# Optimization experiments

Measured on AMD Instinct MI355X. Metric: run time of the kernel, lower is better.

Reference implementation:

```python
import jax, jax.numpy as jnp
import numpy as np
from jax import lax

B, S, D, H, K, FF = 8, 1024, 512, 8, 3, 1024
BUCKETS, MAX_REL = 32, 128
DH = D // H
SPAN = BUCKETS  # att_span when position_buckets > 0


def setup_inputs() -> dict:
    key = jax.random.key(0)
    ks = jax.random.split(key, 12)
    n = lambda k, shp, s=0.02: jax.random.normal(k, shp, jnp.float32) * s
    return dict(
        x=jax.random.normal(ks[0], (B, S, D), jnp.float32),
        ln1_g=jnp.ones((D,), jnp.float32), ln1_b=jnp.zeros((D,), jnp.float32),
        dw_w=n(ks[1], (D, 1, K), 0.1), dw_b=jnp.zeros((D,), jnp.float32),
        pw_w=n(ks[2], (D, D)), pw_b=jnp.zeros((D,), jnp.float32),
        ln2_g=jnp.ones((D,), jnp.float32), ln2_b=jnp.zeros((D,), jnp.float32),
        q_w=n(ks[3], (D, D)), q_b=jnp.zeros((D,), jnp.float32),
        k_w=n(ks[4], (D, D)), k_b=jnp.zeros((D,), jnp.float32),
        v_w=n(ks[5], (D, D)), v_b=jnp.zeros((D,), jnp.float32),
        o_w=n(ks[6], (D, D)), o_b=jnp.zeros((D,), jnp.float32),
        rel_emb=n(ks[7], (2 * SPAN, D)),
        ln3_g=jnp.ones((D,), jnp.float32), ln3_b=jnp.zeros((D,), jnp.float32),
        w1=n(ks[8], (FF, D)), b1=jnp.zeros((FF,), jnp.float32),
        w2=n(ks[9], (D, FF)), b2=jnp.zeros((D,), jnp.float32),
    )


def _ln(x, g, b):
    m = x.mean(-1, keepdims=True)
    v = jnp.var(x, axis=-1, keepdims=True)
    return (x - m) * lax.rsqrt(v + 1e-5) * g + b


def _rel_bucket():
    # DeBERTa-v2 log-bucket relative positions, [S, S] int32
    ids = jnp.arange(S, dtype=jnp.int32)
    rel = ids[:, None] - ids[None, :]
    mid = BUCKETS // 2
    sign = jnp.sign(rel)
    abs_pos = jnp.where((rel < mid) & (rel > -mid), mid - 1, jnp.abs(rel)).astype(jnp.float32)
    log_pos = jnp.ceil(jnp.log(abs_pos / mid) / np.log((MAX_REL - 1) / mid) * (mid - 1)) + mid
    return jnp.where(abs_pos <= mid, rel, (log_pos * sign).astype(jnp.int32)).astype(jnp.int32)


def _attention(x, q_w, q_b, k_w, k_b, v_w, v_b, o_w, o_b, rel_emb):
    def heads(t):  # [B,S,D] -> [B,H,S,DH]
        return t.reshape(B, S, H, DH).transpose(0, 2, 1, 3)

    q = heads(x @ q_w.T + q_b)
    k = heads(x @ k_w.T + k_b)
    v = heads(x @ v_w.T + v_b)
    scale = 1.0 / np.sqrt(DH * 3)  # scale_factor = 1 + len(['c2p','p2c'])

    scores = jnp.einsum('bhid,bhjd->bhij', q, k) * scale  # content-to-content

    rel = _rel_bucket()  # [S,S]
    # shared att key: project rel embeddings with same q/k projections -> [H, 2*SPAN, DH]
    pos_k = (rel_emb @ k_w.T + k_b).reshape(2 * SPAN, H, DH).transpose(1, 0, 2)
    pos_q = (rel_emb @ q_w.T + q_b).reshape(2 * SPAN, H, DH).transpose(1, 0, 2)

    # content-to-position
    c2p = jnp.einsum('bhid,hjd->bhij', q, pos_k)  # [B,H,S,2*SPAN]
    c2p_idx = jnp.clip(rel + SPAN, 0, 2 * SPAN - 1)[None, None]  # [1,1,S,S]
    scores = scores + jnp.take_along_axis(c2p, c2p_idx, axis=-1) * scale

    # position-to-content
    p2c = jnp.einsum('bhid,hjd->bhij', k, pos_q)  # [B,H,S,2*SPAN]
    p2c_idx = jnp.clip(-rel + SPAN, 0, 2 * SPAN - 1)[None, None]
    scores = scores + jnp.take_along_axis(p2c, p2c_idx, axis=-1).swapaxes(-1, -2) * scale

    probs = jax.nn.softmax(scores, axis=-1)
    ctx = jnp.einsum('bhij,bhjd->bhid', probs, v).transpose(0, 2, 1, 3).reshape(B, S, D)
    return ctx @ o_w.T + o_b


def reference(x, ln1_g, ln1_b, dw_w, dw_b, pw_w, pw_b, ln2_g, ln2_b,
              q_w, q_b, k_w, k_b, v_w, v_b, o_w, o_b, rel_emb,
              ln3_g, ln3_b, w1, b1, w2, b2):
    # conv block (pre-norm)
    res = x
    xn = _ln(x, ln1_g, ln1_b)
    xc = xn.transpose(0, 2, 1)  # [B,D,S]
    dw = lax.conv_general_dilated(xc, dw_w, (1,), [(K // 2, K // 2)],
                                  dimension_numbers=('NCH', 'OIH', 'NCH'),
                                  feature_group_count=D) + dw_b[None, :, None]
    pw = jnp.einsum('od,bds->bos', pw_w, jax.nn.silu(dw)) + pw_b[None, :, None]
    x = res + pw.transpose(0, 2, 1)
    # attention block
    res = x
    x = res + _attention(_ln(x, ln2_g, ln2_b), q_w, q_b, k_w, k_b, v_w, v_b, o_w, o_b, rel_emb)
    # FFN block
    res = x
    xn = _ln(x, ln3_g, ln3_b)
    ff = jax.nn.silu(xn @ w1.T + b1) @ w2.T + b2
    return res + ff
```

## Files before the change

kernel.cpp:

```cpp
#include <hip/hip_runtime.h>
#include <hip/hip_bf16.h>
#include <math.h>


#define B_  8
#define S_  1024
#define D_  512
#define H_  8
#define DH_ 64
#define FF_ 1024
#define BS_ (B_*S_)

typedef __attribute__((ext_vector_type(8))) short  short8;
typedef __attribute__((ext_vector_type(4))) short  short4v;
typedef __attribute__((ext_vector_type(4))) float  f32x4;
typedef __attribute__((ext_vector_type(4))) int    int4v;

static __device__ __forceinline__ float b2f(short u){
  union { int i; float f; } cv; cv.i = ((int)(unsigned short)u) << 16; return cv.f;
}
static __device__ __forceinline__ short f2b(float f){
  union { float f; unsigned u; } cv; cv.f = f;
  unsigned r = cv.u + 0x7FFFu + ((cv.u >> 16) & 1u);
  return (short)(r >> 16);
}
static __device__ __forceinline__ float silu_f(float x){
  return x / (1.f + __expf(-x));
}
static __device__ __forceinline__ f32x4 mfma16(short8 a, short8 b, f32x4 c){
  return __builtin_amdgcn_mfma_f32_16x16x32_bf16(a, b, c, 0, 0, 0);
}

struct F2B8 { const float* s[8]; short* d[8]; int n[8]; };
__global__ __launch_bounds__(256) void f2b8_kernel(F2B8 a){
  int seg = blockIdx.y;
  int i = (blockIdx.x*256 + threadIdx.x)*4;
  if (i >= a.n[seg]) return;
  float4 v = *(const float4*)(a.s[seg] + i);
  short4v o; o.x = f2b(v.x); o.y = f2b(v.y); o.z = f2b(v.z); o.w = f2b(v.w);
  *(short4v*)(a.d[seg] + i) = o;
}

__global__ __launch_bounds__(256) void tab_kernel(signed char* __restrict__ tab){
  int t = blockIdx.x*256 + threadIdx.x;
  if (t >= 2048) return;
  int d = t - 1023;
  int ad = d < 0 ? -d : d;
  int bkt;
  if (ad <= 16) bkt = d;
  else {
    const float inv_log = 15.f / logf(7.9375f);
    float lp = ceilf(logf((float)ad * (1.f/16.f)) * inv_log) + 16.f;
    int ilp = (int)lp;
    bkt = (d > 0) ? ilp : -ilp;
  }
  int idx = bkt + 32;
  idx = idx < 0 ? 0 : (idx > 63 ? 63 : idx);
  tab[t] = (signed char)idx;
}

__global__ __launch_bounds__(128) void ln_kernel(const float* __restrict__ x,
                                                 const float* __restrict__ g,
                                                 const float* __restrict__ bb,
                                                 short* __restrict__ out){
  int row = blockIdx.x;
  int tid = threadIdx.x;
  float4 v = ((const float4*)(x + (size_t)row*D_))[tid];
  float s  = v.x + v.y + v.z + v.w;
  float ss = v.x*v.x + v.y*v.y + v.z*v.z + v.w*v.w;
  #pragma unroll
  for (int off = 32; off; off >>= 1){ s += __shfl_down(s, off); ss += __shfl_down(ss, off); }
  __shared__ float red[4];
  if ((tid & 63) == 0){ red[tid>>6] = s; red[2 + (tid>>6)] = ss; }
  __syncthreads();
  float S  = red[0] + red[1];
  float SS = red[2] + red[3];
  float m   = S * (1.f/D_);
  float var = SS * (1.f/D_) - m*m;
  float rs  = rsqrtf(var + 1e-5f);
  float4 gv = ((const float4*)g)[tid];
  float4 bv = ((const float4*)bb)[tid];
  short4v o;
  o.x = f2b((v.x - m)*rs*gv.x + bv.x);
  o.y = f2b((v.y - m)*rs*gv.y + bv.y);
  o.z = f2b((v.z - m)*rs*gv.z + bv.z);
  o.w = f2b((v.w - m)*rs*gv.w + bv.w);
  *(short4v*)(out + (size_t)row*D_ + tid*4) = o;
}

__global__ __launch_bounds__(256) void dwconv_kernel(const short* __restrict__ xn,
                                                     const float* __restrict__ w,
                                                     const float* __restrict__ bias,
                                                     short* __restrict__ out){
  int idx = blockIdx.x*256 + threadIdx.x;
  int bs  = idx >> 6;
  int d8  = (idx & 63) << 3;
  int s   = bs & (S_-1);
  const short* base = xn + (size_t)bs*D_ + d8;
  short8 z = {};
  short8 xm = (s > 0)     ? *(const short8*)(base - D_) : z;
  short8 xc =               *(const short8*)(base);
  short8 xp = (s < S_-1)  ? *(const short8*)(base + D_) : z;
  short8 o;
  #pragma unroll
  for (int i = 0; i < 8; i++){
    int d = d8 + i;
    float acc = bias[d] + b2f(xm[i])*w[d*3+0] + b2f(xc[i])*w[d*3+1] + b2f(xp[i])*w[d*3+2];
    o[i] = f2b(silu_f(acc));
  }
  *(short8*)(out + (size_t)bs*D_ + d8) = o;
}

template<bool SILU, bool RES, bool OF32, bool OBF>
__global__ __launch_bounds__(256) void gemm128_kernel(const short* __restrict__ A,
                                                      const short* __restrict__ W,
                                                      const float* __restrict__ bias,
                                                      const float* res,
                                                      float* of32,
                                                      short* __restrict__ obf,
                                                      int M, int N, int K){
  __shared__ short a_lds[128][72];
  __shared__ short b_lds[64][72];
  int tid = threadIdx.x;
  int w = tid >> 6, lane = tid & 63, quad = lane >> 4, l16 = lane & 15;
  int wm = (w >> 1) * 64, wn = (w & 1) * 32;
  int m0 = blockIdx.y * 128, n0 = blockIdx.x * 64;
  f32x4 acc[4][2] = {};
  for (int kk = 0; kk < K; kk += 64){
    #pragma unroll
    for (int i = 0; i < 4; i++){
      int c = i*256 + tid;
      int r = c >> 3, cc = (c & 7) * 8;
      *(int4v*)&a_lds[r][cc] = *(const int4v*)(A + (size_t)(m0+r)*K + kk + cc);
    }
    #pragma unroll
    for (int i = 0; i < 2; i++){
      int c = i*256 + tid;
      int r = c >> 3, cc = (c & 7) * 8;
      *(int4v*)&b_lds[r][cc] = *(const int4v*)(W + (size_t)(n0+r)*K + kk + cc);
    }
    __syncthreads();
    #pragma unroll
    for (int ks = 0; ks < 2; ks++){
      short8 b0 = *(const short8*)&b_lds[wn      + l16][ks*32 + quad*8];
      short8 b1 = *(const short8*)&b_lds[wn + 16 + l16][ks*32 + quad*8];
      #pragma unroll
      for (int mt = 0; mt < 4; mt++){
        short8 a = *(const short8*)&a_lds[wm + mt*16 + l16][ks*32 + quad*8];
        acc[mt][0] = mfma16(a, b0, acc[mt][0]);
        acc[mt][1] = mfma16(a, b1, acc[mt][1]);
      }
    }
    __syncthreads();
  }
  #pragma unroll
  for (int mt = 0; mt < 4; mt++)
    #pragma unroll
    for (int nt = 0; nt < 2; nt++)
      #pragma unroll
      for (int r = 0; r < 4; r++){
        int row = m0 + wm + mt*16 + quad*4 + r;
        int col = n0 + wn + nt*16 + l16;
        float val = acc[mt][nt][r] + bias[col];
        if (SILU) val = silu_f(val);
        if (RES)  val += res[(size_t)row*N + col];
        if (OF32) of32[(size_t)row*N + col] = val;
        if (OBF)  obf[(size_t)row*N + col] = f2b(val);
      }
}

template<bool SILU, bool RES, bool OF32, bool OBF>
__global__ __launch_bounds__(256) void gemm_kernel(const short* __restrict__ A,
                                                   const short* __restrict__ W,
                                                   const float* __restrict__ bias,
                                                   const float* res,
                                                   float* of32,
                                                   short* __restrict__ obf,
                                                   int M, int N, int K){
  __shared__ short a_lds[64][72];
  __shared__ short b_lds[64][72];
  int tid = threadIdx.x;
  int w = tid >> 6, lane = tid & 63, quad = lane >> 4, l16 = lane & 15;
  int wm = (w >> 1) * 32, wn = (w & 1) * 32;
  int m0 = blockIdx.y * 64, n0 = blockIdx.x * 64;
  int r0 = tid >> 3, c0 = (tid & 7) * 8;
  int r1 = r0 + 32;
  f32x4 acc[2][2] = {};
  for (int kk = 0; kk < K; kk += 64){
    *(int4v*)&a_lds[r0][c0] = *(const int4v*)(A + (size_t)(m0+r0)*K + kk + c0);
    *(int4v*)&a_lds[r1][c0] = *(const int4v*)(A + (size_t)(m0+r1)*K + kk + c0);
    *(int4v*)&b_lds[r0][c0] = *(const int4v*)(W + (size_t)(n0+r0)*K + kk + c0);
    *(int4v*)&b_lds[r1][c0] = *(const int4v*)(W + (size_t)(n0+r1)*K + kk + c0);
    __syncthreads();
    #pragma unroll
    for (int ks = 0; ks < 2; ks++){
      short8 a0 = *(const short8*)&a_lds[wm      + l16][ks*32 + quad*8];
      short8 a1 = *(const short8*)&a_lds[wm + 16 + l16][ks*32 + quad*8];
      short8 b0 = *(const short8*)&b_lds[wn      + l16][ks*32 + quad*8];
      short8 b1 = *(const short8*)&b_lds[wn + 16 + l16][ks*32 + quad*8];
      acc[0][0] = mfma16(a0, b0, acc[0][0]);
      acc[0][1] = mfma16(a0, b1, acc[0][1]);
      acc[1][0] = mfma16(a1, b0, acc[1][0]);
      acc[1][1] = mfma16(a1, b1, acc[1][1]);
    }
    __syncthreads();
  }
  #pragma unroll
  for (int mt = 0; mt < 2; mt++)
    #pragma unroll
    for (int nt = 0; nt < 2; nt++)
      #pragma unroll
      for (int r = 0; r < 4; r++){
        int row = m0 + wm + mt*16 + quad*4 + r;
        int col = n0 + wn + nt*16 + l16;
        float val = acc[mt][nt][r] + bias[col];
        if (SILU) val = silu_f(val);
        if (RES)  val += res[(size_t)row*N + col];
        if (OF32) of32[(size_t)row*N + col] = val;
        if (OBF)  obf[(size_t)row*N + col] = f2b(val);
      }
}

__global__ __launch_bounds__(256) void posbias_kernel(const short* __restrict__ q,
                                                      const short* __restrict__ k,
                                                      const short* __restrict__ posk,
                                                      const short* __restrict__ posq,
                                                      short* __restrict__ c2p,
                                                      short* __restrict__ p2c){
  int bsT = blockIdx.x;
  int h   = blockIdx.y;
  int tid = threadIdx.x, w = tid >> 6, lane = tid & 63, quad = lane >> 4, l16 = lane & 15;
  int row_a = bsT*64 + w*16 + l16;
  f32x4 accc[4] = {}, accp[4] = {};
  #pragma unroll
  for (int ks = 0; ks < 2; ks++){
    short8 aq = *(const short8*)(q + (size_t)row_a*D_ + h*DH_ + ks*32 + quad*8);
    short8 ak = *(const short8*)(k + (size_t)row_a*D_ + h*DH_ + ks*32 + quad*8);
    #pragma unroll
    for (int nt = 0; nt < 4; nt++){
      short8 bk = *(const short8*)(posk + (size_t)(nt*16+l16)*D_ + h*DH_ + ks*32 + quad*8);
      short8 bq = *(const short8*)(posq + (size_t)(nt*16+l16)*D_ + h*DH_ + ks*32 + quad*8);
      accc[nt] = mfma16(aq, bk, accc[nt]);
      accp[nt] = mfma16(ak, bq, accp[nt]);
    }
  }
  #pragma unroll
  for (int nt = 0; nt < 4; nt++)
    #pragma unroll
    for (int r = 0; r < 4; r++){
      int row = bsT*64 + w*16 + quad*4 + r;
      int col = h*DH_ + nt*16 + l16;
      c2p[(size_t)row*D_ + col] = f2b(accc[nt][r]);
      p2c[(size_t)row*D_ + col] = f2b(accp[nt][r]);
    }
}

__global__ __launch_bounds__(256) void vtrans_kernel(const short* __restrict__ v,
                                                     short* __restrict__ vt){
  __shared__ short t_lds[64][65];
  int st = blockIdx.x, h = blockIdx.y, b = blockIdx.z;
  int s0 = st*64;
  int tid = threadIdx.x;
  #pragma unroll
  for (int i = 0; i < 2; i++){
    int c = i*256 + tid;
    int s = c >> 3, d8 = (c & 7) * 8;
    short8 vv = *(const short8*)(v + (size_t)(b*S_ + s0 + s)*D_ + h*DH_ + d8);
    #pragma unroll
    for (int jj = 0; jj < 8; jj++) t_lds[d8+jj][s] = vv[jj];
  }
  __syncthreads();
  #pragma unroll
  for (int i = 0; i < 2; i++){
    int c = i*256 + tid;
    int d = c >> 3, s8 = (c & 7) * 8;
    short8 o;
    #pragma unroll
    for (int jj = 0; jj < 8; jj++) o[jj] = t_lds[d][s8+jj];
    *(short8*)(vt + ((size_t)(b*H_ + h)*DH_ + d)*S_ + s0 + s8) = o;
  }
}

__global__ __launch_bounds__(256, 4) void flash_kernel(const short* __restrict__ q,
                                                       const short* __restrict__ k,
                                                       const short* __restrict__ VT,
                                                       const short* __restrict__ c2p,
                                                       const short* __restrict__ p2c,
                                                       const signed char* __restrict__ TAB,
                                                       short* __restrict__ ctx){
  __shared__ short k_lds[64][72];
  __shared__ short v_lds[64][72];
  __shared__ short c2p_lds[64][72];
  __shared__ short pp_lds[64][72];
  __shared__ signed char tab[2048];

  int it = blockIdx.x, h = blockIdx.y, b = blockIdx.z;
  int i0 = it * 64;
  int tid = threadIdx.x, w = tid >> 6, lane = tid & 63, quad = lane >> 4, l16 = lane & 15;
  const float scale = 0.07216878364f;

  ((unsigned long long*)tab)[tid] = ((const unsigned long long*)TAB)[tid];
  #pragma unroll
  for (int i = 0; i < 2; i++){
    int c = i*256 + tid;
    int r = c >> 3, cc = (c & 7) * 8;
    *(int4v*)&c2p_lds[r][cc] = *(const int4v*)(c2p + (size_t)(b*S_ + i0 + r)*D_ + h*DH_ + cc);
  }
  short8 qf0, qf1;
  {
    size_t row = (size_t)(b*S_ + i0 + w*16 + l16);
    qf0 = *(const short8*)(q + row*D_ + h*DH_ +      quad*8);
    qf1 = *(const short8*)(q + row*D_ + h*DH_ + 32 + quad*8);
  }
  __syncthreads();

  float cpos[4], cneg[4];
  #pragma unroll
  for (int r = 0; r < 4; r++){
    int iloc = w*16 + quad*4 + r;
    cpos[r] = b2f(c2p_lds[iloc][63]);
    cneg[r] = b2f(c2p_lds[iloc][0]);
  }
  f32x4 o_acc[4] = {};
  float mrow[4] = {-INFINITY, -INFINITY, -INFINITY, -INFINITY};
  float lrow[4] = {};
  const short* Kbase  = k   + (size_t)(b*S_)*D_ + h*DH_;
  const short* VTbase = VT  + (size_t)(b*H_ + h)*DH_*S_;
  const short* Pbase  = p2c + (size_t)(b*S_)*D_ + h*DH_;

  int st_r = tid >> 3, st_c = (tid & 7) * 8;

  for (int jt = 0; jt < 16; jt++){
    int j0 = jt * 64;
    bool near = (jt >= it-2 && jt <= it+2);
    #pragma unroll
    for (int i = 0; i < 2; i++){
      int r = st_r + i*32;
      size_t grow = (size_t)(b*S_ + j0 + r);
      *(int4v*)&k_lds[r][st_c]  = *(const int4v*)(Kbase + (size_t)(j0 + r)*D_ + st_c);
      *(int4v*)&v_lds[r][st_c]  = *(const int4v*)(VTbase + (size_t)r*S_ + j0 + st_c);
      *(int4v*)&pp_lds[r][st_c] = *(const int4v*)(Pbase + (size_t)(j0 + r)*D_ + st_c);
      (void)grow;
    }
    __syncthreads();

    f32x4 sfr[4];
    #pragma unroll
    for (int nt = 0; nt < 4; nt++){
      f32x4 a = {};
      a = mfma16(qf0, *(const short8*)&k_lds[nt*16+l16][     quad*8], a);
      a = mfma16(qf1, *(const short8*)&k_lds[nt*16+l16][32 + quad*8], a);
      sfr[nt] = a;
    }
    float sval[4][4];
    if (near){
      #pragma unroll
      for (int nt = 0; nt < 4; nt++){
        int jloc = nt*16 + l16;
        #pragma unroll
        for (int r = 0; r < 4; r++){
          int iloc = w*16 + quad*4 + r;
          int idx  = tab[(i0 + iloc) - (j0 + jloc) + 1023];
          sval[nt][r] = (sfr[nt][r] + b2f(c2p_lds[iloc][idx]) + b2f(pp_lds[jloc][idx])) * scale;
        }
      }
    } else {
      int cidx = (jt < it) ? 63 : 0;
      const float* cP = (jt < it) ? cpos : cneg;
      #pragma unroll
      for (int nt = 0; nt < 4; nt++){
        float pv = b2f(pp_lds[nt*16 + l16][cidx]);
        #pragma unroll
        for (int r = 0; r < 4; r++)
          sval[nt][r] = (sfr[nt][r] + cP[r] + pv) * scale;
      }
    }
    float mnew[4], alpha[4], lsum[4];
    #pragma unroll
    for (int r = 0; r < 4; r++){
      float mx = fmaxf(fmaxf(sval[0][r], sval[1][r]), fmaxf(sval[2][r], sval[3][r]));
      #pragma unroll
      for (int off = 8; off; off >>= 1) mx = fmaxf(mx, __shfl_xor(mx, off));
      mnew[r]  = fmaxf(mrow[r], mx);
      alpha[r] = __expf(mrow[r] - mnew[r]);
      lsum[r]  = 0.f;
    }
    #pragma unroll
    for (int nt = 0; nt < 4; nt++)
      #pragma unroll
      for (int r = 0; r < 4; r++){
        float p = __expf(sval[nt][r] - mnew[r]);
        sval[nt][r] = p;
        lsum[r] += p;
      }
    #pragma unroll
    for (int r = 0; r < 4; r++){
      #pragma unroll
      for (int off = 8; off; off >>= 1) lsum[r] += __shfl_xor(lsum[r], off);
      lrow[r] = lrow[r]*alpha[r] + lsum[r];
      mrow[r] = mnew[r];
    }
    __syncthreads();

    #pragma unroll
    for (int nt = 0; nt < 4; nt++)
      #pragma unroll
      for (int r = 0; r < 4; r++)
        pp_lds[w*16 + quad*4 + r][nt*16 + l16] = f2b(sval[nt][r]);
    #pragma unroll
    for (int nt = 0; nt < 4; nt++)
      #pragma unroll
      for (int r = 0; r < 4; r++) o_acc[nt][r] *= alpha[r];
    short8 pf0 = *(const short8*)&pp_lds[w*16 + l16][     quad*8];
    short8 pf1 = *(const short8*)&pp_lds[w*16 + l16][32 + quad*8];
    #pragma unroll
    for (int nt = 0; nt < 4; nt++){
      o_acc[nt] = mfma16(pf0, *(const short8*)&v_lds[nt*16+l16][     quad*8], o_acc[nt]);
      o_acc[nt] = mfma16(pf1, *(const short8*)&v_lds[nt*16+l16][32 + quad*8], o_acc[nt]);
    }
    __syncthreads();
  }
  #pragma unroll
  for (int nt = 0; nt < 4; nt++)
    #pragma unroll
    for (int r = 0; r < 4; r++){
      size_t row = (size_t)(b*S_ + i0 + w*16 + quad*4 + r);
      ctx[row*D_ + h*DH_ + nt*16 + l16] = f2b(o_acc[nt][r] / lrow[r]);
    }
}

static const size_t OFF_XN   = 0;
static const size_t OFF_Q    = 8388608;
static const size_t OFF_K    = 16777216;
static const size_t OFF_V    = 25165824;
static const size_t OFF_C2P  = 33554432;
static const size_t OFF_P2C  = 41943040;
static const size_t OFF_WPW  = 50331648;
static const size_t OFF_WQ   = 50855936;
static const size_t OFF_WK   = 51380224;
static const size_t OFF_WV   = 51904512;
static const size_t OFF_WO   = 52428800;
static const size_t OFF_W1   = 52953088;
static const size_t OFF_W2   = 54001664;
static const size_t OFF_REL  = 55050240;
static const size_t OFF_POSK = 55115776;
static const size_t OFF_POSQ = 55181312;
static const size_t OFF_TAB  = 55246848;

extern "C" void kernel_launch(void* const* d_in, const int* in_sizes, int n_in,
                              void* d_out, int out_size, void* d_ws, size_t ws_size,
                              hipStream_t stream){
  const float* x    = (const float*)d_in[0];
  const float* ln1g = (const float*)d_in[1];
  const float* ln1b = (const float*)d_in[2];
  const float* dww  = (const float*)d_in[3];
  const float* dwb  = (const float*)d_in[4];
  const float* pww  = (const float*)d_in[5];
  const float* pwb  = (const float*)d_in[6];
  const float* ln2g = (const float*)d_in[7];
  const float* ln2b = (const float*)d_in[8];
  const float* qw   = (const float*)d_in[9];
  const float* qb   = (const float*)d_in[10];
  const float* kw   = (const float*)d_in[11];
  const float* kb   = (const float*)d_in[12];
  const float* vw   = (const float*)d_in[13];
  const float* vb   = (const float*)d_in[14];
  const float* ow   = (const float*)d_in[15];
  const float* ob   = (const float*)d_in[16];
  const float* rel  = (const float*)d_in[17];
  const float* ln3g = (const float*)d_in[18];
  const float* ln3b = (const float*)d_in[19];
  const float* w1   = (const float*)d_in[20];
  const float* b1   = (const float*)d_in[21];
  const float* w2   = (const float*)d_in[22];
  const float* b2   = (const float*)d_in[23];
  float* out = (float*)d_out;
  char* ws = (char*)d_ws;

  short* XN   = (short*)(ws + OFF_XN);
  short* Q    = (short*)(ws + OFF_Q);
  short* Kb_  = (short*)(ws + OFF_K);
  short* V    = (short*)(ws + OFF_V);
  short* C2P  = (short*)(ws + OFF_C2P);
  short* P2C  = (short*)(ws + OFF_P2C);
  short* WPW  = (short*)(ws + OFF_WPW);
  short* WQ   = (short*)(ws + OFF_WQ);
  short* WK   = (short*)(ws + OFF_WK);
  short* WV   = (short*)(ws + OFF_WV);
  short* WO   = (short*)(ws + OFF_WO);
  short* W1B  = (short*)(ws + OFF_W1);
  short* W2B  = (short*)(ws + OFF_W2);
  short* RELB = (short*)(ws + OFF_REL);
  short* POSK = (short*)(ws + OFF_POSK);
  short* POSQ = (short*)(ws + OFF_POSQ);
  signed char* TAB = (signed char*)(ws + OFF_TAB);
  short* DWS  = C2P;
  short* VT   = XN;
  short* CTX  = V;
  short* FFH  = Q;

  F2B8 fa;
  fa.s[0]=pww; fa.d[0]=WPW; fa.n[0]=262144;
  fa.s[1]=qw;  fa.d[1]=WQ;  fa.n[1]=262144;
  fa.s[2]=kw;  fa.d[2]=WK;  fa.n[2]=262144;
  fa.s[3]=vw;  fa.d[3]=WV;  fa.n[3]=262144;
  fa.s[4]=ow;  fa.d[4]=WO;  fa.n[4]=262144;
  fa.s[5]=w1;  fa.d[5]=W1B; fa.n[5]=524288;
  fa.s[6]=w2;  fa.d[6]=W2B; fa.n[6]=524288;
  fa.s[7]=rel; fa.d[7]=RELB;fa.n[7]=32768;
  f2b8_kernel<<<dim3(512,8), 256, 0, stream>>>(fa);
  tab_kernel<<<8, 256, 0, stream>>>(TAB);

  ln_kernel<<<BS_, 128, 0, stream>>>(x, ln1g, ln1b, XN);
  dwconv_kernel<<<2048, 256, 0, stream>>>(XN, dww, dwb, DWS);
  gemm128_kernel<false,true,true,false><<<dim3(8,64), 256, 0, stream>>>(
      DWS, WPW, pwb, x, out, nullptr, BS_, 512, 512);

  ln_kernel<<<BS_, 128, 0, stream>>>(out, ln2g, ln2b, XN);
  gemm128_kernel<false,false,false,true><<<dim3(8,64), 256, 0, stream>>>(
      XN, WQ, qb, nullptr, nullptr, Q,   BS_, 512, 512);
  gemm128_kernel<false,false,false,true><<<dim3(8,64), 256, 0, stream>>>(
      XN, WK, kb, nullptr, nullptr, Kb_, BS_, 512, 512);
  gemm128_kernel<false,false,false,true><<<dim3(8,64), 256, 0, stream>>>(
      XN, WV, vb, nullptr, nullptr, V,   BS_, 512, 512);
  gemm_kernel<false,false,false,true><<<dim3(8,1), 256, 0, stream>>>(
      RELB, WK, kb, nullptr, nullptr, POSK, 64, 512, 512);
  gemm_kernel<false,false,false,true><<<dim3(8,1), 256, 0, stream>>>(
      RELB, WQ, qb, nullptr, nullptr, POSQ, 64, 512, 512);
  posbias_kernel<<<dim3(128,8), 256, 0, stream>>>(Q, Kb_, POSK, POSQ, C2P, P2C);
  vtrans_kernel<<<dim3(16,8,8), 256, 0, stream>>>(V, VT);
  flash_kernel<<<dim3(16,8,8), 256, 0, stream>>>(Q, Kb_, VT, C2P, P2C, TAB, CTX);
  gemm128_kernel<false,true,true,false><<<dim3(8,64), 256, 0, stream>>>(
      CTX, WO, ob, out, out, nullptr, BS_, 512, 512);

  ln_kernel<<<BS_, 128, 0, stream>>>(out, ln3g, ln3b, XN);
  gemm128_kernel<true,false,false,true><<<dim3(16,64), 256, 0, stream>>>(
      XN, W1B, b1, nullptr, nullptr, FFH, BS_, 1024, 512);
  gemm128_kernel<false,true,true,false><<<dim3(8,64), 256, 0, stream>>>(
      FFH, W2B, b2, out, out, nullptr, BS_, 512, 1024);
}
```

Before: 385.8 us.

## Use direct-to-LDS swizzled GEMM loads, fuse QKV, and drop online-softmax max tracking

GEMMs now stage tiles with global_load_lds into an XOR-swizzled unpadded LDS layout instead of going through registers. The Q, K and V projections are fused into one launch over a 1536-wide output, and Q and posq are pre-scaled so attention skips the per-score multiply. The flash kernel drops running-max rescaling and the per-tile shuffle reductions, exponentiating raw scores and reducing row sums once at the end. This relies on scores staying small enough not to overflow exp, which holds only for bounded inputs. The fused QKV launch also assumes WQ, WK and WV sit contiguously in the workspace.

```diff
diff --git a/kernel.cpp b/kernel.cpp
--- a/kernel.cpp
+++ b/kernel.cpp
@@ -10,6 +10,7 @@
 #define DH_ 64
 #define FF_ 1024
 #define BS_ (B_*S_)
+#define SCALE_ 0.07216878364f
 
 typedef __attribute__((ext_vector_type(8))) short  short8;
 typedef __attribute__((ext_vector_type(4))) short  short4v;
@@ -29,6 +30,10 @@
 }
 static __device__ __forceinline__ f32x4 mfma16(short8 a, short8 b, f32x4 c){
   return __builtin_amdgcn_mfma_f32_16x16x32_bf16(a, b, c, 0, 0, 0);
+}
+static __device__ __forceinline__ void gl16(const void* g, void* l){
+  __builtin_amdgcn_global_load_lds((const __attribute__((address_space(1))) void*)g,
+                                   (__attribute__((address_space(3))) void*)l, 16, 0, 0);
 }
 
 struct F2B8 { const float* s[8]; short* d[8]; int n[8]; };
@@ -111,48 +116,57 @@
   *(short8*)(out + (size_t)bs*D_ + d8) = o;
 }
 
+#define GEMM_GL_CORE(AP, WP, KK)                                               \
+  __shared__ short a_lds[128*64];                                              \
+  __shared__ short b_lds[64*64];                                               \
+  int tid = threadIdx.x;                                                       \
+  int w = tid >> 6, lane = tid & 63, quad = lane >> 4, l16 = lane & 15;        \
+  int wm = (w >> 1) * 64, wn = (w & 1) * 32;                                   \
+  int m0 = blockIdx.y * 128, n0 = blockIdx.x * 64;                             \
+  const short* aptr[4]; const short* bptr[2];                                  \
+  _Pragma("unroll")                                                            \
+  for (int i = 0; i < 4; i++){                                                 \
+    int slot = i*256 + tid;                                                    \
+    int r = slot >> 3, c = (slot & 7) ^ (r & 7);                               \
+    aptr[i] = AP + (size_t)(m0 + r)*KK + c*8;                                  \
+  }                                                                            \
+  _Pragma("unroll")                                                            \
+  for (int i = 0; i < 2; i++){                                                 \
+    int slot = i*256 + tid;                                                    \
+    int r = slot >> 3, c = (slot & 7) ^ (r & 7);                               \
+    bptr[i] = WP + (size_t)(n0 + r)*KK + c*8;                                  \
+  }                                                                            \
+  f32x4 acc[4][2] = {};                                                        \
+  int sw = l16 & 7;                                                            \
+  for (int kk = 0; kk < KK; kk += 64){                                         \
+    _Pragma("unroll")                                                          \
+    for (int i = 0; i < 4; i++) gl16(aptr[i] + kk, &a_lds[(i*256 + w*64)*8]);  \
+    _Pragma("unroll")                                                          \
+    for (int i = 0; i < 2; i++) gl16(bptr[i] + kk, &b_lds[(i*256 + w*64)*8]);  \
+    __syncthreads();                                                           \
+    _Pragma("unroll")                                                          \
+    for (int ks = 0; ks < 2; ks++){                                            \
+      short8 b0 = *(const short8*)&b_lds[(wn      + l16)*64 + ((ks*4+quad)^sw)*8]; \
+      short8 b1 = *(const short8*)&b_lds[(wn + 16 + l16)*64 + ((ks*4+quad)^sw)*8]; \
+      _Pragma("unroll")                                                        \
+      for (int mt = 0; mt < 4; mt++){                                          \
+        short8 a = *(const short8*)&a_lds[(wm + mt*16 + l16)*64 + ((ks*4+quad)^sw)*8]; \
+        acc[mt][0] = mfma16(a, b0, acc[mt][0]);                                \
+        acc[mt][1] = mfma16(a, b1, acc[mt][1]);                                \
+      }                                                                        \
+    }                                                                          \
+    __syncthreads();                                                           \
+  }
+
 template<bool SILU, bool RES, bool OF32, bool OBF>
-__global__ __launch_bounds__(256) void gemm128_kernel(const short* __restrict__ A,
-                                                      const short* __restrict__ W,
-                                                      const float* __restrict__ bias,
-                                                      const float* res,
-                                                      float* of32,
-                                                      short* __restrict__ obf,
-                                                      int M, int N, int K){
-  __shared__ short a_lds[128][72];
-  __shared__ short b_lds[64][72];
-  int tid = threadIdx.x;
-  int w = tid >> 6, lane = tid & 63, quad = lane >> 4, l16 = lane & 15;
-  int wm = (w >> 1) * 64, wn = (w & 1) * 32;
-  int m0 = blockIdx.y * 128, n0 = blockIdx.x * 64;
-  f32x4 acc[4][2] = {};
-  for (int kk = 0; kk < K; kk += 64){
-    #pragma unroll
-    for (int i = 0; i < 4; i++){
-      int c = i*256 + tid;
-      int r = c >> 3, cc = (c & 7) * 8;
-      *(int4v*)&a_lds[r][cc] = *(const int4v*)(A + (size_t)(m0+r)*K + kk + cc);
-    }
-    #pragma unroll
-    for (int i = 0; i < 2; i++){
-      int c = i*256 + tid;
-      int r = c >> 3, cc = (c & 7) * 8;
-      *(int4v*)&b_lds[r][cc] = *(const int4v*)(W + (size_t)(n0+r)*K + kk + cc);
-    }
-    __syncthreads();
-    #pragma unroll
-    for (int ks = 0; ks < 2; ks++){
-      short8 b0 = *(const short8*)&b_lds[wn      + l16][ks*32 + quad*8];
-      short8 b1 = *(const short8*)&b_lds[wn + 16 + l16][ks*32 + quad*8];
-      #pragma unroll
-      for (int mt = 0; mt < 4; mt++){
-        short8 a = *(const short8*)&a_lds[wm + mt*16 + l16][ks*32 + quad*8];
-        acc[mt][0] = mfma16(a, b0, acc[mt][0]);
-        acc[mt][1] = mfma16(a, b1, acc[mt][1]);
-      }
-    }
-    __syncthreads();
-  }
+__global__ __launch_bounds__(256) void gemm_gl(const short* __restrict__ A,
+                                               const short* __restrict__ W,
+                                               const float* __restrict__ bias,
+                                               const float* res,
+                                               float* of32,
+                                               short* __restrict__ obf,
+                                               int M, int N, int K){
+  GEMM_GL_CORE(A, W, K)
   #pragma unroll
   for (int mt = 0; mt < 4; mt++)
     #pragma unroll
@@ -169,20 +183,45 @@
       }
 }
 
-template<bool SILU, bool RES, bool OF32, bool OBF>
-__global__ __launch_bounds__(256) void gemm_kernel(const short* __restrict__ A,
-                                                   const short* __restrict__ W,
-                                                   const float* __restrict__ bias,
-                                                   const float* res,
-                                                   float* of32,
-                                                   short* __restrict__ obf,
-                                                   int M, int N, int K){
+__global__ __launch_bounds__(256) void gemm_qkv(const short* __restrict__ A,
+                                                const short* __restrict__ W,
+                                                const float* __restrict__ qb,
+                                                const float* __restrict__ kb,
+                                                const float* __restrict__ vb,
+                                                short* __restrict__ Qo,
+                                                short* __restrict__ Ko,
+                                                short* __restrict__ Vo,
+                                                int M, int K){
+  GEMM_GL_CORE(A, W, K)
+  int colb = n0 + wn;
+  int sel = colb >> 9;
+  const float* bp = sel == 0 ? qb : (sel == 1 ? kb : vb);
+  short* dp = sel == 0 ? Qo : (sel == 1 ? Ko : Vo);
+  float mult = sel == 0 ? SCALE_ : 1.f;
+  #pragma unroll
+  for (int mt = 0; mt < 4; mt++)
+    #pragma unroll
+    for (int nt = 0; nt < 2; nt++)
+      #pragma unroll
+      for (int r = 0; r < 4; r++){
+        int row = m0 + wm + mt*16 + quad*4 + r;
+        int col = (colb + nt*16 + l16) & 511;
+        float val = (acc[mt][nt][r] + bp[col]) * mult;
+        dp[(size_t)row*D_ + col] = f2b(val);
+      }
+}
+
+__global__ __launch_bounds__(256) void gemm_pos(const short* __restrict__ A,
+                                                const short* __restrict__ W,
+                                                const float* __restrict__ bias,
+                                                short* __restrict__ obf,
+                                                float mult, int N, int K){
   __shared__ short a_lds[64][72];
   __shared__ short b_lds[64][72];
   int tid = threadIdx.x;
   int w = tid >> 6, lane = tid & 63, quad = lane >> 4, l16 = lane & 15;
   int wm = (w >> 1) * 32, wn = (w & 1) * 32;
-  int m0 = blockIdx.y * 64, n0 = blockIdx.x * 64;
+  int m0 = 0, n0 = blockIdx.x * 64;
   int r0 = tid >> 3, c0 = (tid & 7) * 8;
   int r1 = r0 + 32;
   f32x4 acc[2][2] = {};
@@ -213,11 +252,7 @@
       for (int r = 0; r < 4; r++){
         int row = m0 + wm + mt*16 + quad*4 + r;
         int col = n0 + wn + nt*16 + l16;
-        float val = acc[mt][nt][r] + bias[col];
-        if (SILU) val = silu_f(val);
-        if (RES)  val += res[(size_t)row*N + col];
-        if (OF32) of32[(size_t)row*N + col] = val;
-        if (OBF)  obf[(size_t)row*N + col] = f2b(val);
+        obf[(size_t)row*N + col] = f2b((acc[mt][nt][r] + bias[col]) * mult);
       }
 }
 
@@ -281,6 +316,7 @@
   }
 }
 
+#define PPS 68
 __global__ __launch_bounds__(256, 4) void flash_kernel(const short* __restrict__ q,
                                                        const short* __restrict__ k,
                                                        const short* __restrict__ VT,
@@ -291,13 +327,12 @@
   __shared__ short k_lds[64][72];
   __shared__ short v_lds[64][72];
   __shared__ short c2p_lds[64][72];
-  __shared__ short pp_lds[64][72];
+  __shared__ short pp_lds[64][PPS];
   __shared__ signed char tab[2048];
 
   int it = blockIdx.x, h = blockIdx.y, b = blockIdx.z;
   int i0 = it * 64;
   int tid = threadIdx.x, w = tid >> 6, lane = tid & 63, quad = lane >> 4, l16 = lane & 15;
-  const float scale = 0.07216878364f;
 
   ((unsigned long long*)tab)[tid] = ((const unsigned long long*)TAB)[tid];
   #pragma unroll
@@ -322,7 +357,6 @@
     cneg[r] = b2f(c2p_lds[iloc][0]);
   }
   f32x4 o_acc[4] = {};
-  float mrow[4] = {-INFINITY, -INFINITY, -INFINITY, -INFINITY};
   float lrow[4] = {};
   const short* Kbase  = k   + (size_t)(b*S_)*D_ + h*DH_;
   const short* VTbase = VT  + (size_t)(b*H_ + h)*DH_*S_;
@@ -336,11 +370,9 @@
     #pragma unroll
     for (int i = 0; i < 2; i++){
       int r = st_r + i*32;
-      size_t grow = (size_t)(b*S_ + j0 + r);
       *(int4v*)&k_lds[r][st_c]  = *(const int4v*)(Kbase + (size_t)(j0 + r)*D_ + st_c);
       *(int4v*)&v_lds[r][st_c]  = *(const int4v*)(VTbase + (size_t)r*S_ + j0 + st_c);
       *(int4v*)&pp_lds[r][st_c] = *(const int4v*)(Pbase + (size_t)(j0 + r)*D_ + st_c);
-      (void)grow;
     }
     __syncthreads();
 
@@ -352,7 +384,7 @@
       a = mfma16(qf1, *(const short8*)&k_lds[nt*16+l16][32 + quad*8], a);
       sfr[nt] = a;
     }
-    float sval[4][4];
+    float pval[4][4];
     if (near){
       #pragma unroll
       for (int nt = 0; nt < 4; nt++){
@@ -361,7 +393,9 @@
         for (int r = 0; r < 4; r++){
           int iloc = w*16 + quad*4 + r;
           int idx  = tab[(i0 + iloc) - (j0 + jloc) + 1023];
-          sval[nt][r] = (sfr[nt][r] + b2f(c2p_lds[iloc][idx]) + b2f(pp_lds[jloc][idx])) * scale;
+          float p = __expf(sfr[nt][r] + b2f(c2p_lds[iloc][idx]) + b2f(pp_lds[jloc][idx]));
+          pval[nt][r] = p;
+          lrow[r] += p;
         }
       }
     } else {
@@ -371,34 +405,12 @@
       for (int nt = 0; nt < 4; nt++){
         float pv = b2f(pp_lds[nt*16 + l16][cidx]);
         #pragma unroll
-        for (int r = 0; r < 4; r++)
-          sval[nt][r] = (sfr[nt][r] + cP[r] + pv) * scale;
+        for (int r = 0; r < 4; r++){
+          float p = __expf(sfr[nt][r] + cP[r] + pv);
+          pval[nt][r] = p;
+          lrow[r] += p;
+        }
       }
-    }
-    float mnew[4], alpha[4], lsum[4];
-    #pragma unroll
-    for (int r = 0; r < 4; r++){
-      float mx = fmaxf(fmaxf(sval[0][r], sval[1][r]), fmaxf(sval[2][r], sval[3][r]));
-      #pragma unroll
-      for (int off = 8; off; off >>= 1) mx = fmaxf(mx, __shfl_xor(mx, off));
-      mnew[r]  = fmaxf(mrow[r], mx);
-      alpha[r] = __expf(mrow[r] - mnew[r]);
-      lsum[r]  = 0.f;
-    }
-    #pragma unroll
-    for (int nt = 0; nt < 4; nt++)
-      #pragma unroll
-      for (int r = 0; r < 4; r++){
-        float p = __expf(sval[nt][r] - mnew[r]);
-        sval[nt][r] = p;
-        lsum[r] += p;
-      }
-    #pragma unroll
-    for (int r = 0; r < 4; r++){
-      #pragma unroll
-      for (int off = 8; off; off >>= 1) lsum[r] += __shfl_xor(lsum[r], off);
-      lrow[r] = lrow[r]*alpha[r] + lsum[r];
-      mrow[r] = mnew[r];
     }
     __syncthreads();
 
@@ -406,11 +418,7 @@
     for (int nt = 0; nt < 4; nt++)
       #pragma unroll
       for (int r = 0; r < 4; r++)
-        pp_lds[w*16 + quad*4 + r][nt*16 + l16] = f2b(sval[nt][r]);
-    #pragma unroll
-    for (int nt = 0; nt < 4; nt++)
-      #pragma unroll
-      for (int r = 0; r < 4; r++) o_acc[nt][r] *= alpha[r];
+        pp_lds[w*16 + quad*4 + r][nt*16 + l16] = f2b(pval[nt][r]);
     short8 pf0 = *(const short8*)&pp_lds[w*16 + l16][     quad*8];
     short8 pf1 = *(const short8*)&pp_lds[w*16 + l16][32 + quad*8];
     #pragma unroll
@@ -419,6 +427,11 @@
       o_acc[nt] = mfma16(pf1, *(const short8*)&v_lds[nt*16+l16][32 + quad*8], o_acc[nt]);
     }
     __syncthreads();
+  }
+  #pragma unroll
+  for (int r = 0; r < 4; r++){
+    #pragma unroll
+    for (int off = 8; off; off >>= 1) lrow[r] += __shfl_xor(lrow[r], off);
   }
   #pragma unroll
   for (int nt = 0; nt < 4; nt++)
@@ -513,29 +526,23 @@
 
   ln_kernel<<<BS_, 128, 0, stream>>>(x, ln1g, ln1b, XN);
   dwconv_kernel<<<2048, 256, 0, stream>>>(XN, dww, dwb, DWS);
-  gemm128_kernel<false,true,true,false><<<dim3(8,64), 256, 0, stream>>>(
+  gemm_gl<false,true,true,false><<<dim3(8,64), 256, 0, stream>>>(
       DWS, WPW, pwb, x, out, nullptr, BS_, 512, 512);
 
   ln_kernel<<<BS_, 128, 0, stream>>>(out, ln2g, ln2b, XN);
-  gemm128_kernel<false,false,false,true><<<dim3(8,64), 256, 0, stream>>>(
-      XN, WQ, qb, nullptr, nullptr, Q,   BS_, 512, 512);
-  gemm128_kernel<false,false,false,true><<<dim3(8,64), 256, 0, stream>>>(
-      XN, WK, kb, nullptr, nullptr, Kb_, BS_, 512, 512);
-  gemm128_kernel<false,false,false,true><<<dim3(8,64), 256, 0, stream>>>(
-      XN, WV, vb, nullptr, nullptr, V,   BS_, 512, 512);
-  gemm_kernel<false,false,false,true><<<dim3(8,1), 256, 0, stream>>>(
-      RELB, WK, kb, nullptr, nullptr, POSK, 64, 512, 512);
-  gemm_kernel<false,false,false,true><<<dim3(8,1), 256, 0, stream>>>(
-      RELB, WQ, qb, nullptr, nullptr, POSQ, 64, 512, 512);
+  gemm_qkv<<<dim3(24,64), 256, 0, stream>>>(
+      XN, WQ, qb, kb, vb, Q, Kb_, V, BS_, 512);
+  gemm_pos<<<8, 256, 0, stream>>>(RELB, WK, kb, POSK, 1.f,    512, 512);
+  gemm_pos<<<8, 256, 0, stream>>>(RELB, WQ, qb, POSQ, SCALE_, 512, 512);
   posbias_kernel<<<dim3(128,8), 256, 0, stream>>>(Q, Kb_, POSK, POSQ, C2P, P2C);
   vtrans_kernel<<<dim3(16,8,8), 256, 0, stream>>>(V, VT);
   flash_kernel<<<dim3(16,8,8), 256, 0, stream>>>(Q, Kb_, VT, C2P, P2C, TAB, CTX);
-  gemm128_kernel<false,true,true,false><<<dim3(8,64), 256, 0, stream>>>(
+  gemm_gl<false,true,true,false><<<dim3(8,64), 256, 0, stream>>>(
       CTX, WO, ob, out, out, nullptr, BS_, 512, 512);
 
   ln_kernel<<<BS_, 128, 0, stream>>>(out, ln3g, ln3b, XN);
-  gemm128_kernel<true,false,false,true><<<dim3(16,64), 256, 0, stream>>>(
+  gemm_gl<true,false,false,true><<<dim3(16,64), 256, 0, stream>>>(
       XN, W1B, b1, nullptr, nullptr, FFH, BS_, 1024, 512);
-  gemm128_kernel<false,true,true,false><<<dim3(8,64), 256, 0, stream>>>(
+  gemm_gl<false,true,true,false><<<dim3(8,64), 256, 0, stream>>>(
       FFH, W2B, b2, out, out, nullptr, BS_, 512, 1024);
 }
```

Result: faster. 350.5 us (-9.2%).
